# Kernel optimization log

Measured on AMD Instinct MI355X. Metric: run time of the kernel, lower is better.

## Reference

```python
import jax, jax.numpy as jnp
import numpy as np

HIDDEN = 1024

def setup_inputs() -> dict:
    key = jax.random.key(0)
    ks = jax.random.split(key, 4)
    scale = 1.0 / np.sqrt(HIDDEN)
    return {
        "X": jax.random.normal(ks[0], (4, 4096, HIDDEN), dtype=jnp.float32),
        "Wq": jax.random.normal(ks[1], (HIDDEN, HIDDEN), dtype=jnp.float32) * scale,
        "bq": jnp.zeros((HIDDEN,), dtype=jnp.float32),
        "Wk": jax.random.normal(ks[2], (HIDDEN, HIDDEN), dtype=jnp.float32) * scale,
        "bk": jnp.zeros((HIDDEN,), dtype=jnp.float32),
        "Wv": jax.random.normal(ks[3], (HIDDEN, HIDDEN), dtype=jnp.float32) * scale,
        "bv": jnp.zeros((HIDDEN,), dtype=jnp.float32),
    }

def reference(X, Wq, bq, Wk, bk, Wv, bv):
    # nn.Linear: x @ W.T + b
    Q = jnp.einsum("bsh,dh->bsd", X, Wq) + bq   # [B,S,H]
    K = jnp.einsum("bsh,dh->bsd", X, Wk) + bk
    V = jnp.einsum("bsh,dh->bsd", X, Wv) + bv
    scores = jnp.einsum("bsd,btd->bst", Q, K) / jnp.sqrt(jnp.asarray(X.shape[-1], X.dtype))  # [B,S,S]
    attn = jax.nn.softmax(scores, axis=-1)
    return jnp.einsum("bst,btd->bsd", attn, V)  # [B,S,H]
```

## Files before the change

### kernel.cpp

```cpp
#include <hip/hip_runtime.h>
#include <math.h>

#define HIDDEN 1024
#define SEQ    4096
#define BATCH  4

typedef _Float16 f16x8 __attribute__((ext_vector_type(8)));
typedef float    floatx4 __attribute__((ext_vector_type(4)));

__device__ inline void gld16(const void* g, void* l) {
    __builtin_amdgcn_global_load_lds(
        (const __attribute__((address_space(1))) unsigned int*)g,
        (__attribute__((address_space(3))) unsigned int*)l, 16, 0, 0);
}

template<int MODE, int NT>
__global__ __launch_bounds__(512)
void gemm256_kernel(const _Float16* __restrict__ A,
                    const _Float16* __restrict__ Bq,
                    const _Float16* __restrict__ Bk,
                    const _Float16* __restrict__ Bv,
                    const float* __restrict__ bq,
                    const float* __restrict__ bk,
                    const float* __restrict__ bv,
                    float alpha,
                    _Float16* __restrict__ Eo,
                    _Float16* __restrict__ Qo,
                    _Float16* __restrict__ Ko,
                    _Float16* __restrict__ Vo,
                    float* __restrict__ Cf,
                    float* __restrict__ Lsum) {
    constexpr int LDAB = (MODE == 4) ? SEQ : HIDDEN;
    __shared__ __align__(16) char smem[131072];
    char* sA = smem;
    char* sB = smem + 65536;

    const int tid  = threadIdx.x;
    const int lane = tid & 63;
    const int w    = tid >> 6;
    const int wm   = w & 1;
    const int wn   = w >> 1;
    const int quad = lane >> 4;
    const int l16  = lane & 15;
    const int swz  = (l16 >> 1) & 3;

    int row0, col0, z = 0;
    if constexpr (MODE == 5) {
        const int n = blockIdx.x, xcd = n & 7, slot = n >> 3;
        const int cc = slot % 12, rg = xcd + 8 * (slot / 12);
        row0 = rg * 256; col0 = cc * 256;
    } else if constexpr (MODE == 3) {
        z = blockIdx.y;
        const int bx = blockIdx.x, wgid = (bx & 7) * 32 + (bx >> 3);
        row0 = (wgid >> 4) * 256; col0 = (wgid & 15) * 256;
    } else {
        z = blockIdx.y;
        const int n = blockIdx.x, xcd = n & 7, slot = n >> 3;
        const int cc = slot & 3, rg = xcd + 8 * (slot >> 2);
        row0 = rg * 256; col0 = cc * 256;
    }

    const _Float16* Abase;
    const _Float16* Bbase;
    int colbase = col0, which = 0;
    if constexpr (MODE == 5) {
        which = col0 >> 10; colbase = col0 & 1023;
        const _Float16* Bsrc = (which == 0) ? Bq : (which == 1) ? Bk : Bv;
        Abase = A + (size_t)row0 * HIDDEN;
        Bbase = Bsrc + (size_t)colbase * HIDDEN;
    } else if constexpr (MODE == 3) {
        Abase = A  + (size_t)z * SEQ * HIDDEN + (size_t)row0 * HIDDEN;
        Bbase = Bq + (size_t)z * SEQ * HIDDEN + (size_t)col0 * HIDDEN;
        Eo   += (size_t)z * SEQ * SEQ;
        Lsum += (size_t)z * SEQ;
    } else {
        Abase = A  + (size_t)z * SEQ * SEQ    + (size_t)row0 * SEQ;
        Bbase = Bq + (size_t)z * HIDDEN * SEQ + (size_t)col0 * SEQ;
        Cf   += (size_t)z * SEQ * HIDDEN;
        Lsum += (size_t)z * SEQ;
    }

    const int n0 = tid, n1 = tid + 512;
    const int r0s = n0 >> 2, p0s = n0 & 3;
    const int r1s = n1 >> 2, p1s = n1 & 3;
    const int off0 = r0s * LDAB + (p0s ^ ((r0s >> 1) & 3)) * 8;
    const int off1 = r1s * LDAB + (p1s ^ ((r1s >> 1) & 3)) * 8;

    auto stage = [&](const _Float16* base, char* lh, int kt, int kh) {
        const int kb = kt * 64 + kh * 32;
        gld16(base + off0 + kb, lh + n0 * 16);
        gld16(base + off1 + kb, lh + n1 * 16);
    };

    floatx4 acc[8][4];
    #pragma unroll
    for (int i = 0; i < 8; ++i)
        #pragma unroll
        for (int j = 0; j < 4; ++j) acc[i][j] = (floatx4){0.f, 0.f, 0.f, 0.f};

    f16x8 afA[4], afB[4], bfX[4], bfY[4];

#define RD_AF(DST, RH, KH, B_)                                                \
  { const f16x8* pAh = (const f16x8*)(sA + ((B_) * 2 + (KH)) * 16384);        \
    _Pragma("unroll")                                                         \
    for (int i = 0; i < 4; ++i)                                               \
      DST[i] = pAh[(wm * 128 + (RH) * 64 + i * 16 + l16) * 4 + (quad ^ swz)]; }

#define RD_BF(DST, KH, B_)                                                    \
  { const f16x8* pBh = (const f16x8*)(sB + ((B_) * 2 + (KH)) * 16384);        \
    _Pragma("unroll")                                                         \
    for (int j = 0; j < 4; ++j)                                               \
      DST[j] = pBh[(wn * 64 + j * 16 + l16) * 4 + (quad ^ swz)]; }

#define MM(RH, AF, BF)                                                        \
  __builtin_amdgcn_sched_barrier(0);                                          \
  __builtin_amdgcn_s_setprio(1);                                              \
  _Pragma("unroll")                                                           \
  for (int j = 0; j < 4; ++j)                                                 \
    _Pragma("unroll")                                                         \
    for (int i = 0; i < 4; ++i)                                               \
      acc[(RH) * 4 + i][j] = __builtin_amdgcn_mfma_f32_16x16x32_f16(          \
          AF[i], BF[j], acc[(RH) * 4 + i][j], 0, 0, 0);                       \
  __builtin_amdgcn_s_setprio(0);

#define QK_TILE(T_, S01, S23, W0S, W2S, RDNEXT)                               \
  { const int b_ = (T_) & 1, nb_ = b_ ^ 1;                                    \
                                                            \
    __builtin_amdgcn_s_barrier();                                             \
    RD_AF(afB, 1, 0, b_);                                                     \
    if (S01) stage(Abase, sA + (nb_ * 2 + 1) * 16384, (T_) + 1, 1);           \
    MM(0, afA, bfX)                                                           \
    asm volatile("s_waitcnt vmcnt(" W0S ")" ::: "memory");                    \
                                                            \
    __builtin_amdgcn_s_barrier();                                             \
    RD_AF(afA, 0, 1, b_);                                                     \
    RD_BF(bfY, 1, b_);                                                        \
    if (S01) stage(Bbase, sB + (nb_ * 2 + 1) * 16384, (T_) + 1, 1);           \
    MM(1, afB, bfX)                                                           \
                                                            \
    __builtin_amdgcn_s_barrier();                                             \
    RD_AF(afB, 1, 1, b_);                                                     \
    if (S23) stage(Abase, sA + (b_ * 2 + 0) * 16384, (T_) + 2, 0);            \
    MM(0, afA, bfY)                                                           \
    if (RDNEXT) asm volatile("s_waitcnt vmcnt(" W2S ")" ::: "memory");        \
                                                            \
    __builtin_amdgcn_s_barrier();                                             \
    if (RDNEXT) {                                                             \
      RD_AF(afA, 0, 0, nb_);                                                  \
      RD_BF(bfX, 0, nb_);                                                     \
    }                                                                         \
    if (S23) stage(Bbase, sB + (b_ * 2 + 0) * 16384, (T_) + 2, 0);            \
    MM(1, afB, bfY)                                                           \
  }

    stage(Abase, sA + 0 * 16384, 0, 0);
    stage(Bbase, sB + 0 * 16384, 0, 0);
    stage(Abase, sA + 1 * 16384, 0, 1);
    stage(Bbase, sB + 1 * 16384, 0, 1);
    stage(Abase, sA + 2 * 16384, 1, 0);
    stage(Bbase, sB + 2 * 16384, 1, 0);
    asm volatile("s_waitcnt vmcnt(8)" ::: "memory");
    __builtin_amdgcn_s_barrier();
    RD_AF(afA, 0, 0, 0);
    RD_BF(bfX, 0, 0);

    #pragma unroll 2
    for (int t = 0; t < NT - 2; ++t) QK_TILE(t, 1, 1, "6", "6", 1)
    QK_TILE(NT - 2, 1, 0, "6", "4", 1)
    QK_TILE(NT - 1, 0, 0, "0", "0", 0)

#undef QK_TILE
#undef MM
#undef RD_BF
#undef RD_AF

    #pragma unroll
    for (int i = 0; i < 8; ++i) {
        const int r0 = row0 + wm * 128 + i * 16 + quad * 4;
        if constexpr (MODE == 3) {
            float rp[4] = {0.f, 0.f, 0.f, 0.f};
            #pragma unroll
            for (int j = 0; j < 4; ++j) {
                const int cl = col0 + wn * 64 + j * 16 + l16;
                #pragma unroll
                for (int reg = 0; reg < 4; ++reg) {
                    const float v = exp2f(alpha * acc[i][j][reg] - 5.770780163555856f);
                    const _Float16 vh = (_Float16)v;
                    Eo[(size_t)(r0 + reg) * SEQ + cl] = vh;
                    rp[reg] += (float)vh;
                }
            }
            #pragma unroll
            for (int off = 1; off < 16; off <<= 1)
                #pragma unroll
                for (int reg = 0; reg < 4; ++reg)
                    rp[reg] += __shfl_xor(rp[reg], off, 64);
            if (l16 == 0)
                #pragma unroll
                for (int reg = 0; reg < 4; ++reg)
                    atomicAdd(&Lsum[r0 + reg], rp[reg]);
        } else if constexpr (MODE == 5) {
            #pragma unroll
            for (int j = 0; j < 4; ++j) {
                const int cl = colbase + wn * 64 + j * 16 + l16;
                const float bcol = (which == 0 ? bq : which == 1 ? bk : bv)[cl];
                if (which < 2) {
                    _Float16* O = (which == 0) ? Qo : Ko;
                    #pragma unroll
                    for (int reg = 0; reg < 4; ++reg)
                        O[(size_t)(r0 + reg) * HIDDEN + cl] =
                            (_Float16)(acc[i][j][reg] + bcol);
                } else {
                    const int bb = r0 >> 12;
                    const int s  = r0 & 4095;
                    _Float16 tq[4];
                    #pragma unroll
                    for (int reg = 0; reg < 4; ++reg)
                        tq[reg] = (_Float16)(acc[i][j][reg] + bcol);
                    *(uint2*)&Vo[((size_t)bb * HIDDEN + cl) * SEQ + s] = *(const uint2*)tq;
                }
            }
        } else {
            float linv[4];
            #pragma unroll
            for (int reg = 0; reg < 4; ++reg) linv[reg] = 1.0f / Lsum[r0 + reg];
            #pragma unroll
            for (int j = 0; j < 4; ++j) {
                const int cl = col0 + wn * 64 + j * 16 + l16;
                #pragma unroll
                for (int reg = 0; reg < 4; ++reg)
                    Cf[(size_t)(r0 + reg) * HIDDEN + cl] = acc[i][j][reg] * linv[reg];
            }
        }
    }
}

__global__ __launch_bounds__(256)
void cast_x_kernel(const float* __restrict__ in, _Float16* __restrict__ out) {
    const int i = blockIdx.x * 256 + threadIdx.x;
    const float4 x = ((const float4*)in)[i];
    _Float16 h[4] = {(_Float16)x.x, (_Float16)x.y, (_Float16)x.z, (_Float16)x.w};
    ((uint2*)out)[i] = *(const uint2*)h;
}

__global__ __launch_bounds__(256)
void cast_w_kernel(const float* __restrict__ w0, const float* __restrict__ w1,
                   const float* __restrict__ w2,
                   _Float16* __restrict__ o0, _Float16* __restrict__ o1,
                   _Float16* __restrict__ o2) {
    const float* in = (blockIdx.z == 0) ? w0 : (blockIdx.z == 1) ? w1 : w2;
    _Float16* out   = (blockIdx.z == 0) ? o0 : (blockIdx.z == 1) ? o1 : o2;
    const int i = blockIdx.x * 256 + threadIdx.x;
    const float4 x = ((const float4*)in)[i];
    _Float16 h[4] = {(_Float16)x.x, (_Float16)x.y, (_Float16)x.z, (_Float16)x.w};
    ((uint2*)out)[i] = *(const uint2*)h;
}

extern "C" void kernel_launch(void* const* d_in, const int* in_sizes, int n_in,
                              void* d_out, int out_size, void* d_ws, size_t ws_size,
                              hipStream_t stream) {
    const float* X  = (const float*)d_in[0];
    const float* Wq = (const float*)d_in[1];
    const float* bq = (const float*)d_in[2];
    const float* Wk = (const float*)d_in[3];
    const float* bk = (const float*)d_in[4];
    const float* Wv = (const float*)d_in[5];
    const float* bv = (const float*)d_in[6];
    float* out = (float*)d_out;

    char* ws = (char*)d_ws;
    const size_t EB = (size_t)BATCH * SEQ * SEQ * 2;
    const size_t XB = (size_t)BATCH * SEQ * HIDDEN * 2;
    const size_t WB = (size_t)HIDDEN * HIDDEN * 2;

    _Float16* E   = (_Float16*)ws;
    _Float16* Xh  = (_Float16*)ws;
    _Float16* Wqh = (_Float16*)(ws + XB);
    _Float16* Wkh = (_Float16*)(ws + XB + WB);
    _Float16* Wvh = (_Float16*)(ws + XB + 2 * WB);
    _Float16* Qh  = (_Float16*)(ws + EB);
    _Float16* Kh  = (_Float16*)(ws + EB + XB);
    _Float16* Vt  = (_Float16*)(ws + EB + 2 * XB);
    float*    Lsum= (float*)   (ws + EB + 3 * XB);

    cast_x_kernel<<<dim3(16384), dim3(256), 0, stream>>>(X, Xh);
    cast_w_kernel<<<dim3(1024, 1, 3), dim3(256), 0, stream>>>(
        Wq, Wk, Wv, Wqh, Wkh, Wvh);

    hipMemsetAsync(Lsum, 0, (size_t)BATCH * SEQ * sizeof(float), stream);

    gemm256_kernel<5, 16><<<dim3(768), dim3(512), 0, stream>>>(
        Xh, Wqh, Wkh, Wvh, bq, bk, bv, 0.f,
        nullptr, Qh, Kh, Vt, nullptr, nullptr);

    const float alpha2 = (1.0f / 32.0f) * 1.4426950408889634f;
    gemm256_kernel<3, 16><<<dim3(256, 4), dim3(512), 0, stream>>>(
        Qh, Kh, nullptr, nullptr, nullptr, nullptr, nullptr, alpha2,
        E, nullptr, nullptr, nullptr, nullptr, Lsum);

    gemm256_kernel<4, 64><<<dim3(64, 4), dim3(512), 0, stream>>>(
        E, Vt, nullptr, nullptr, nullptr, nullptr, nullptr, 0.f,
        nullptr, nullptr, nullptr, nullptr, out, Lsum);
}
```

Baseline: 527.0 us.

## Shrink GEMM K-tile to 32 with simple double-buffered pipeline

Replaces the 64-wide K tile, split into two 32-halves with a multi-barrier software pipeline, with a 32-wide K tile and a plain double buffer. Each iteration does a full vmcnt(0) wait and one barrier, then issues the next tile's loads during the MFMAs. Shared memory use halves to 64 KB, which may let two blocks share a CU, and the iteration counts double to cover the same K. The price is less prefetch depth and a full wait on global loads every iteration, which can expose memory latency.

```diff
diff --git a/kernel.cpp b/kernel.cpp
--- a/kernel.cpp
+++ b/kernel.cpp
@@ -31,9 +31,9 @@
                     float* __restrict__ Cf,
                     float* __restrict__ Lsum) {
     constexpr int LDAB = (MODE == 4) ? SEQ : HIDDEN;
-    __shared__ __align__(16) char smem[131072];
+    __shared__ __align__(16) char smem[65536];
     char* sA = smem;
-    char* sB = smem + 65536;
+    char* sB = smem + 32768;
 
     const int tid  = threadIdx.x;
     const int lane = tid & 63;
@@ -86,8 +86,8 @@
     const int off0 = r0s * LDAB + (p0s ^ ((r0s >> 1) & 3)) * 8;
     const int off1 = r1s * LDAB + (p1s ^ ((r1s >> 1) & 3)) * 8;
 
-    auto stage = [&](const _Float16* base, char* lh, int kt, int kh) {
-        const int kb = kt * 64 + kh * 32;
+    auto stage = [&](const _Float16* base, char* lh, int kt) {
+        const int kb = kt * 32;
         gld16(base + off0 + kb, lh + n0 * 16);
         gld16(base + off1 + kb, lh + n1 * 16);
     };
@@ -98,16 +98,16 @@
         #pragma unroll
         for (int j = 0; j < 4; ++j) acc[i][j] = (floatx4){0.f, 0.f, 0.f, 0.f};
 
-    f16x8 afA[4], afB[4], bfX[4], bfY[4];
-
-#define RD_AF(DST, RH, KH, B_)                                                \
-  { const f16x8* pAh = (const f16x8*)(sA + ((B_) * 2 + (KH)) * 16384);        \
+    f16x8 afA[4], afB[4], bfX[4];
+
+#define RD_AF(DST, RH, B_)                                                    \
+  { const f16x8* pAh = (const f16x8*)(sA + (B_) * 16384);                     \
     _Pragma("unroll")                                                         \
     for (int i = 0; i < 4; ++i)                                               \
       DST[i] = pAh[(wm * 128 + (RH) * 64 + i * 16 + l16) * 4 + (quad ^ swz)]; }
 
-#define RD_BF(DST, KH, B_)                                                    \
-  { const f16x8* pBh = (const f16x8*)(sB + ((B_) * 2 + (KH)) * 16384);        \
+#define RD_BF(DST, B_)                                                        \
+  { const f16x8* pBh = (const f16x8*)(sB + (B_) * 16384);                     \
     _Pragma("unroll")                                                         \
     for (int j = 0; j < 4; ++j)                                               \
       DST[j] = pBh[(wn * 64 + j * 16 + l16) * 4 + (quad ^ swz)]; }
@@ -123,53 +123,27 @@
           AF[i], BF[j], acc[(RH) * 4 + i][j], 0, 0, 0);                       \
   __builtin_amdgcn_s_setprio(0);
 
-#define QK_TILE(T_, S01, S23, W0S, W2S, RDNEXT)                               \
+#define QTILE(T_, STG)                                                        \
   { const int b_ = (T_) & 1, nb_ = b_ ^ 1;                                    \
-                                                            \
+    asm volatile("s_waitcnt vmcnt(0)" ::: "memory");                          \
     __builtin_amdgcn_s_barrier();                                             \
-    RD_AF(afB, 1, 0, b_);                                                     \
-    if (S01) stage(Abase, sA + (nb_ * 2 + 1) * 16384, (T_) + 1, 1);           \
+    RD_AF(afA, 0, b_);                                                        \
+    RD_BF(bfX, b_);                                                           \
+    RD_AF(afB, 1, b_);                                                        \
+    if (STG) stage(Abase, sA + nb_ * 16384, (T_) + 1);                        \
     MM(0, afA, bfX)                                                           \
-    asm volatile("s_waitcnt vmcnt(" W0S ")" ::: "memory");                    \
-                                                            \
-    __builtin_amdgcn_s_barrier();                                             \
-    RD_AF(afA, 0, 1, b_);                                                     \
-    RD_BF(bfY, 1, b_);                                                        \
-    if (S01) stage(Bbase, sB + (nb_ * 2 + 1) * 16384, (T_) + 1, 1);           \
+    if (STG) stage(Bbase, sB + nb_ * 16384, (T_) + 1);                        \
     MM(1, afB, bfX)                                                           \
-                                                            \
-    __builtin_amdgcn_s_barrier();                                             \
-    RD_AF(afB, 1, 1, b_);                                                     \
-    if (S23) stage(Abase, sA + (b_ * 2 + 0) * 16384, (T_) + 2, 0);            \
-    MM(0, afA, bfY)                                                           \
-    if (RDNEXT) asm volatile("s_waitcnt vmcnt(" W2S ")" ::: "memory");        \
-                                                            \
-    __builtin_amdgcn_s_barrier();                                             \
-    if (RDNEXT) {                                                             \
-      RD_AF(afA, 0, 0, nb_);                                                  \
-      RD_BF(bfX, 0, nb_);                                                     \
-    }                                                                         \
-    if (S23) stage(Bbase, sB + (b_ * 2 + 0) * 16384, (T_) + 2, 0);            \
-    MM(1, afB, bfY)                                                           \
   }
 
-    stage(Abase, sA + 0 * 16384, 0, 0);
-    stage(Bbase, sB + 0 * 16384, 0, 0);
-    stage(Abase, sA + 1 * 16384, 0, 1);
-    stage(Bbase, sB + 1 * 16384, 0, 1);
-    stage(Abase, sA + 2 * 16384, 1, 0);
-    stage(Bbase, sB + 2 * 16384, 1, 0);
-    asm volatile("s_waitcnt vmcnt(8)" ::: "memory");
-    __builtin_amdgcn_s_barrier();
-    RD_AF(afA, 0, 0, 0);
-    RD_BF(bfX, 0, 0);
+    stage(Abase, sA, 0);
+    stage(Bbase, sB, 0);
 
     #pragma unroll 2
-    for (int t = 0; t < NT - 2; ++t) QK_TILE(t, 1, 1, "6", "6", 1)
-    QK_TILE(NT - 2, 1, 0, "6", "4", 1)
-    QK_TILE(NT - 1, 0, 0, "0", "0", 0)
-
-#undef QK_TILE
+    for (int t = 0; t < NT - 1; ++t) QTILE(t, 1)
+    QTILE(NT - 1, 0)
+
+#undef QTILE
 #undef MM
 #undef RD_BF
 #undef RD_AF
@@ -289,16 +263,16 @@
 
     hipMemsetAsync(Lsum, 0, (size_t)BATCH * SEQ * sizeof(float), stream);
 
-    gemm256_kernel<5, 16><<<dim3(768), dim3(512), 0, stream>>>(
+    gemm256_kernel<5, 32><<<dim3(768), dim3(512), 0, stream>>>(
         Xh, Wqh, Wkh, Wvh, bq, bk, bv, 0.f,
         nullptr, Qh, Kh, Vt, nullptr, nullptr);
 
     const float alpha2 = (1.0f / 32.0f) * 1.4426950408889634f;
-    gemm256_kernel<3, 16><<<dim3(256, 4), dim3(512), 0, stream>>>(
+    gemm256_kernel<3, 32><<<dim3(256, 4), dim3(512), 0, stream>>>(
         Qh, Kh, nullptr, nullptr, nullptr, nullptr, nullptr, alpha2,
         E, nullptr, nullptr, nullptr, nullptr, Lsum);
 
-    gemm256_kernel<4, 64><<<dim3(64, 4), dim3(512), 0, stream>>>(
+    gemm256_kernel<4, 128><<<dim3(64, 4), dim3(512), 0, stream>>>(
         E, Vt, nullptr, nullptr, nullptr, nullptr, nullptr, 0.f,
         nullptr, nullptr, nullptr, nullptr, out, Lsum);
 }
```

After: 518.9 us. No clear change (-1.5%).
